# Kernel tuning notes

Measured on AMD Instinct MI355X. Metric: run time of the kernel, lower is better.

The kernel has to match this reference:

```python
import jax, jax.numpy as jnp
import numpy as np

B, N, NP, NS = 8, 4096, 1024, 32
CF = 64            # input point-feature channels; in_channel = 3 + CF = 67
MLP = [64, 128, 256]
EPS = 1e-5         # BatchNorm eps (torch default)


def setup_inputs() -> dict:
    key = jax.random.key(0)
    ks = jax.random.split(key, 8)
    inp = {
        "xyz": jax.random.normal(ks[0], (B, N, 3), jnp.float32),
        "points": jax.random.normal(ks[1], (B, CF, N), jnp.float32),
        "sample_idx": jax.random.randint(ks[2], (B, NP), 0, N, dtype=jnp.int32),
        "neighbor_idx": jax.random.randint(ks[3], (B, NP, NS), 0, N, dtype=jnp.int32),
    }
    c = 3 + CF
    for i, o in enumerate(MLP):
        wk = jax.random.fold_in(ks[4], i)
        inp[f"W{i}"] = jax.random.normal(wk, (o, c), jnp.float32) * (1.0 / np.sqrt(c))
        inp[f"b{i}"] = jnp.zeros((o,), jnp.float32)
        inp[f"gamma{i}"] = jnp.ones((o,), jnp.float32)
        inp[f"beta{i}"] = jnp.zeros((o,), jnp.float32)
        c = o
    return inp


def _forward(xyz, points, sample_idx, neighbor_idx, params):
    # xyz: (B,N,3)  points: (B,CF,N)
    new_xyz = jnp.take_along_axis(xyz, sample_idx[:, :, None], axis=1)        # (B,NP,3)
    nbr_xyz = jax.vmap(lambda x, idx: x[idx])(xyz, neighbor_idx)               # (B,NP,NS,3)
    rel = nbr_xyz - new_xyz[:, :, None, :]                                     # (B,NP,NS,3)
    nbr_feat = jax.vmap(lambda f, idx: f[:, idx])(points, neighbor_idx)        # (B,CF,NP,NS)
    x = jnp.concatenate([rel.transpose(0, 3, 1, 2), nbr_feat], axis=1)         # (B,3+CF,NP,NS)
    # 1x1 Conv2d -> BatchNorm2d (training-mode batch stats) -> ReLU stack
    for W, b, g, be in params:
        x = jnp.einsum('oc,bcps->bops', W, x) + b[None, :, None, None]
        mu = x.mean(axis=(0, 2, 3), keepdims=True)
        var = x.var(axis=(0, 2, 3), keepdims=True)
        x = g[None, :, None, None] * (x - mu) * jax.lax.rsqrt(var + EPS) + be[None, :, None, None]
        x = jax.nn.relu(x)
    new_points = x.max(axis=-1)                                                # (B,C_out,NP)
    return new_xyz, new_points


def reference(xyz, points, sample_idx, neighbor_idx,
              W0, b0, gamma0, beta0,
              W1, b1, gamma1, beta1,
              W2, b2, gamma2, beta2):
    params = [(W0, b0, gamma0, beta0), (W1, b1, gamma1, beta1), (W2, b2, gamma2, beta2)]
    return _forward(xyz, points, sample_idx, neighbor_idx, params)
```

## Files before the change

### kernel.cpp

```cpp
#include <hip/hip_runtime.h>

typedef unsigned short u16;
typedef unsigned int u32;
typedef __attribute__((ext_vector_type(8))) short short8;
typedef __attribute__((ext_vector_type(4))) float f32x4;

#define BB 8
#define NN 4096
#define NPP 1024
#define NSS 32
#define CFF 64
#define C0 67
#define H0 64
#define H1 128
#define H2 256
#define MTOT (BB*NPP*NSS)
#define BN_EPS 1e-5f
#define INV_M (1.0f/262144.0f)

#define MFMA16(a,b,c) __builtin_amdgcn_mfma_f32_16x16x32_bf16(a,b,c,0,0,0)

__device__ __forceinline__ float bf2f(u16 h){ return __uint_as_float(((u32)h)<<16); }
__device__ __forceinline__ u16 f2bf(float f){
  u32 u = __float_as_uint(f);
  u32 r = (u + 0x7fffu + ((u>>16)&1u)) >> 16;
  return (u16)r;
}
__device__ __forceinline__ u32 pack2(float a, float b){
  return (u32)f2bf(a) | ((u32)f2bf(b)<<16);
}

#define WS_NEED 46280704u

__global__ __launch_bounds__(256) void k_setup(
    const float* __restrict__ xyz, const float* __restrict__ points,
    const int* __restrict__ sidx,
    const float* __restrict__ W0, const float* __restrict__ W1, const float* __restrict__ W2,
    u16* __restrict__ ptsT, u16* __restrict__ Wt0c, u16* __restrict__ Wt1c,
    u16* __restrict__ Wt2c, float* __restrict__ out_newxyz)
{
  int blk = blockIdx.x, tid = threadIdx.x;
  if (blk < 512) {
    __shared__ float t[64][65];
    int b = blk >> 6, n0 = (blk & 63) << 6;
    int nloc = tid & 63, cpart = tid >> 6;
    for (int i = 0; i < 16; ++i) {
      int c = i*4 + cpart;
      t[c][nloc] = points[(size_t)(b*CFF + c)*NN + n0 + nloc];
    }
    __syncthreads();
    int cloc = tid & 63, npart = tid >> 6;
    for (int i = 0; i < 16; ++i) {
      int n = i*4 + npart;
      ptsT[((size_t)(b*NN + n0 + n))*CFF + cloc] = f2bf(t[cloc][n]);
    }
  } else if (blk < 544) {
    int t0 = (blk - 512)*256 + tid;
    int b = t0 >> 10;
    int s = sidx[t0];
    for (int k = 0; k < 3; ++k)
      out_newxyz[(size_t)t0*3 + k] = xyz[((size_t)(b*NN + s))*3 + k];
  } else if (blk == 544) {
    for (int i = 0; i < 24; ++i) {
      int e = i*256 + tid;
      int kc = e >> 9, o = (e >> 3) & 63, j = e & 7, k = kc*8 + j;
      float v = (k < 64) ? W0[o*C0 + 3 + k] : ((k < 67) ? W0[o*C0 + (k - 64)] : 0.f);
      Wt0c[e] = f2bf(v);
    }
  } else if (blk == 545) {
    for (int i = 0; i < 32; ++i) {
      int e = i*256 + tid;
      int kc = e >> 10, n = (e >> 3) & 127, j = e & 7;
      Wt1c[e] = f2bf(W1[n*H0 + kc*8 + j]);
    }
  } else {
    int base = (blk - 546) * 4096;
    for (int i = 0; i < 16; ++i) {
      int e = base + i*256 + tid;
      int kc = e >> 11, n = (e >> 3) & 255, j = e & 7;
      Wt2c[e] = f2bf(W2[n*H1 + kc*8 + j]);
    }
  }
}

__global__ __launch_bounds__(256) void k_xyz_only(
    const float* __restrict__ xyz, const int* __restrict__ sidx, float* __restrict__ out_newxyz)
{
  int t0 = blockIdx.x*256 + threadIdx.x;
  int b = t0 >> 10;
  int s = sidx[t0];
  for (int k = 0; k < 3; ++k)
    out_newxyz[(size_t)t0*3 + k] = xyz[((size_t)(b*NN + s))*3 + k];
}

__global__ __launch_bounds__(256) void k_l0(
    const float* __restrict__ xyz, const int* __restrict__ sidx, const int* __restrict__ nidx,
    const u16* __restrict__ ptsT, const u16* __restrict__ Wt0c,
    u16* __restrict__ y0, float* __restrict__ stats)
{
  __shared__ u16 XLc[12*512];
  __shared__ u16 W0c[12*512];
  int tid = threadIdx.x;
  int m0 = blockIdx.x * 64;
  int b = m0 >> 15;

  for (int i = 0; i < 3; ++i)
    ((uint4*)W0c)[i*256 + tid] = ((const uint4*)Wt0c)[i*256 + tid];

  int pos = tid & 63, grp = tid >> 6;
  int m = m0 + pos;
  int nb = nidx[m];
  {
    const u16* prow = ptsT + ((size_t)(b*NN + nb))*CFF + grp*16;
    uint4 h0 = *(const uint4*)prow;
    uint4 h1 = *(const uint4*)(prow + 8);
    *(uint4*)&XLc[(2*grp)*512 + pos*8]   = h0;
    *(uint4*)&XLc[(2*grp+1)*512 + pos*8] = h1;
    if (grp == 0) {
      int p = (m & 32767) >> 5;
      int sp = sidx[b*NPP + p];
      float r0 = xyz[((size_t)(b*NN+nb))*3+0] - xyz[((size_t)(b*NN+sp))*3+0];
      float r1 = xyz[((size_t)(b*NN+nb))*3+1] - xyz[((size_t)(b*NN+sp))*3+1];
      float r2 = xyz[((size_t)(b*NN+nb))*3+2] - xyz[((size_t)(b*NN+sp))*3+2];
      uint4 v = { pack2(r0, r1), pack2(r2, 0.f), 0u, 0u };
      *(uint4*)&XLc[8*512 + pos*8] = v;
    } else {
      uint4 z = {0u,0u,0u,0u};
      *(uint4*)&XLc[(8+grp)*512 + pos*8] = z;
    }
  }
  __syncthreads();

  int lane = tid & 63, wv = tid >> 6;
  int quad = lane >> 4, l15 = lane & 15;
  f32x4 acc0[4];
  for (int mi = 0; mi < 4; ++mi) acc0[mi] = (f32x4){0.f,0.f,0.f,0.f};

  for (int kc = 0; kc < 3; ++kc) {
    int cb = kc*4 + quad;
    short8 bfrag = *(const short8*)&W0c[(cb*64 + wv*16 + l15)*8];
    for (int mi = 0; mi < 4; ++mi) {
      short8 afrag = *(const short8*)&XLc[(cb*64 + mi*16 + l15)*8];
      acc0[mi] = MFMA16(afrag, bfrag, acc0[mi]);
    }
  }

  float s = 0.f, q = 0.f;
  for (int mi = 0; mi < 4; ++mi)
    for (int r = 0; r < 4; ++r) { float y = acc0[mi][r]; s += y; q += y*y; }
  s += __shfl_xor(s, 16); s += __shfl_xor(s, 32);
  q += __shfl_xor(q, 16); q += __shfl_xor(q, 32);
  if (lane < 16) {
    int slot = blockIdx.x & 7;
    atomicAdd(&stats[slot*256 + wv*16 + lane], s);
    atomicAdd(&stats[2048 + slot*256 + wv*16 + lane], q);
  }
  for (int mi = 0; mi < 4; ++mi)
    for (int r = 0; r < 4; ++r) {
      int row = m0 + mi*16 + quad*4 + r;
      y0[(size_t)row*H0 + wv*16 + l15] = f2bf(acc0[mi][r]);
    }
}

__global__ __launch_bounds__(256) void k_l1s(
    const u16* __restrict__ y0, const u16* __restrict__ Wt1c,
    const float* __restrict__ g0, const float* __restrict__ e0,
    const float* __restrict__ stIn, float* __restrict__ stOut)
{
  __shared__ u16 X0c[8*512];
  __shared__ u16 W1c[8*1024];
  __shared__ float scl0[64], sft0[64];
  int tid = threadIdx.x;
  int m0 = blockIdx.x * 64;

  if (tid < 64) {
    float s = 0.f, q = 0.f;
    for (int sl = 0; sl < 8; ++sl) { s += stIn[sl*256 + tid]; q += stIn[2048 + sl*256 + tid]; }
    float mu = s*INV_M, var = q*INV_M - mu*mu;
    float sc = g0[tid] * rsqrtf(var + BN_EPS);
    scl0[tid] = sc; sft0[tid] = e0[tid] - mu*sc;
  }
  for (int i = 0; i < 4; ++i)
    ((uint4*)W1c)[i*256 + tid] = ((const uint4*)Wt1c)[i*256 + tid];

  int pos = tid & 63, grp = tid >> 6;
  {
    const u16* row = y0 + (size_t)(m0 + pos)*H0 + grp*16;
    u16 hs[16];
    *(uint4*)&hs[0] = *(const uint4*)row;
    *(uint4*)&hs[8] = *(const uint4*)(row + 8);
    __syncthreads();
    u16 ob[16];
    for (int j = 0; j < 16; ++j) {
      int c = grp*16 + j;
      ob[j] = f2bf(fmaxf(fmaf(scl0[c], bf2f(hs[j]), sft0[c]), 0.f));
    }
    *(uint4*)&X0c[(2*grp)*512 + pos*8]   = *(uint4*)&ob[0];
    *(uint4*)&X0c[(2*grp+1)*512 + pos*8] = *(uint4*)&ob[8];
  }
  __syncthreads();

  int lane = tid & 63, wv = tid >> 6, quad = lane >> 4, l15 = lane & 15;
  f32x4 acc1[2][4];
  for (int ni = 0; ni < 2; ++ni) for (int mi = 0; mi < 4; ++mi) acc1[ni][mi] = (f32x4){0.f,0.f,0.f,0.f};

  for (int kc = 0; kc < 2; ++kc) {
    int cb = kc*4 + quad;
    short8 a[4], bfr[2];
    for (int mi = 0; mi < 4; ++mi) a[mi] = *(const short8*)&X0c[(cb*64 + mi*16 + l15)*8];
    for (int ni = 0; ni < 2; ++ni) bfr[ni] = *(const short8*)&W1c[(cb*128 + wv*32 + ni*16 + l15)*8];
    for (int ni = 0; ni < 2; ++ni)
      for (int mi = 0; mi < 4; ++mi)
        acc1[ni][mi] = MFMA16(a[mi], bfr[ni], acc1[ni][mi]);
  }

  int slot = blockIdx.x & 7;
  for (int ni = 0; ni < 2; ++ni) {
    float s = 0.f, q = 0.f;
    for (int mi = 0; mi < 4; ++mi)
      for (int r = 0; r < 4; ++r) { float y = acc1[ni][mi][r]; s += y; q += y*y; }
    s += __shfl_xor(s, 16); s += __shfl_xor(s, 32);
    q += __shfl_xor(q, 16); q += __shfl_xor(q, 32);
    if (lane < 16) {
      atomicAdd(&stOut[slot*256 + wv*32 + ni*16 + lane], s);
      atomicAdd(&stOut[2048 + slot*256 + wv*32 + ni*16 + lane], q);
    }
  }
}

__global__ __launch_bounds__(256) void k_l2f(
    const u16* __restrict__ y0, const u16* __restrict__ Wt1c, const u16* __restrict__ Wt2c,
    const float* __restrict__ g0, const float* __restrict__ e0,
    const float* __restrict__ g1, const float* __restrict__ e1,
    const float* __restrict__ st0, const float* __restrict__ st1, float* __restrict__ stOut,
    u16* __restrict__ mxp, u16* __restrict__ mnp)
{
  __shared__ u16 X1c[16*512];
  __shared__ u16 UB[16*1024];
  __shared__ float scl0[64], sft0[64], scl1[128], sft1[128];
  int tid = threadIdx.x;
  int m0 = blockIdx.x * 64;

  if (tid < 64) {
    float s = 0.f, q = 0.f;
    for (int sl = 0; sl < 8; ++sl) { s += st0[sl*256 + tid]; q += st0[2048 + sl*256 + tid]; }
    float mu = s*INV_M, var = q*INV_M - mu*mu;
    float sc = g0[tid] * rsqrtf(var + BN_EPS);
    scl0[tid] = sc; sft0[tid] = e0[tid] - mu*sc;
  }
  if (tid < 128) {
    float s = 0.f, q = 0.f;
    for (int sl = 0; sl < 8; ++sl) { s += st1[sl*256 + tid]; q += st1[2048 + sl*256 + tid]; }
    float mu = s*INV_M, var = q*INV_M - mu*mu;
    float sc = g1[tid] * rsqrtf(var + BN_EPS);
    scl1[tid] = sc; sft1[tid] = e1[tid] - mu*sc;
  }
  u16* X0c = UB;
  u16* W1c = UB + 4096;
  for (int i = 0; i < 4; ++i)
    ((uint4*)W1c)[i*256 + tid] = ((const uint4*)Wt1c)[i*256 + tid];

  int pos = tid & 63, grp = tid >> 6;
  {
    const u16* row = y0 + (size_t)(m0 + pos)*H0 + grp*16;
    u16 hs[16];
    *(uint4*)&hs[0] = *(const uint4*)row;
    *(uint4*)&hs[8] = *(const uint4*)(row + 8);
    __syncthreads();
    u16 ob[16];
    for (int j = 0; j < 16; ++j) {
      int c = grp*16 + j;
      ob[j] = f2bf(fmaxf(fmaf(scl0[c], bf2f(hs[j]), sft0[c]), 0.f));
    }
    *(uint4*)&X0c[(2*grp)*512 + pos*8]   = *(uint4*)&ob[0];
    *(uint4*)&X0c[(2*grp+1)*512 + pos*8] = *(uint4*)&ob[8];
  }
  __syncthreads();

  int lane = tid & 63, wv = tid >> 6, quad = lane >> 4, l15 = lane & 15;
  f32x4 acc1[2][4];
  for (int ni = 0; ni < 2; ++ni) for (int mi = 0; mi < 4; ++mi) acc1[ni][mi] = (f32x4){0.f,0.f,0.f,0.f};

  for (int kc = 0; kc < 2; ++kc) {
    int cb = kc*4 + quad;
    short8 a[4], bfr[2];
    for (int mi = 0; mi < 4; ++mi) a[mi] = *(const short8*)&X0c[(cb*64 + mi*16 + l15)*8];
    for (int ni = 0; ni < 2; ++ni) bfr[ni] = *(const short8*)&W1c[(cb*128 + wv*32 + ni*16 + l15)*8];
    for (int ni = 0; ni < 2; ++ni)
      for (int mi = 0; mi < 4; ++mi)
        acc1[ni][mi] = MFMA16(a[mi], bfr[ni], acc1[ni][mi]);
  }
  __syncthreads();

  for (int ni = 0; ni < 2; ++ni)
    for (int mi = 0; mi < 4; ++mi)
      for (int r = 0; r < 4; ++r) {
        int ch = wv*32 + ni*16 + l15;
        int mm = mi*16 + quad*4 + r;
        float v = fmaxf(fmaf(scl1[ch], acc1[ni][mi][r], sft1[ch]), 0.f);
        X1c[(ch >> 3)*512 + mm*8 + (ch & 7)] = f2bf(v);
      }

  f32x4 acc2[4][4];
  for (int ni = 0; ni < 4; ++ni) for (int mi = 0; mi < 4; ++mi) acc2[ni][mi] = (f32x4){0.f,0.f,0.f,0.f};

  for (int h = 0; h < 2; ++h) {
    for (int i = 0; i < 8; ++i)
      ((uint4*)UB)[i*256 + tid] = ((const uint4*)(Wt2c + h*16384))[i*256 + tid];
    __syncthreads();
    for (int kc = 0; kc < 2; ++kc) {
      int cb = kc*4 + quad;
      int cx = h*8 + cb;
      short8 a[4], bfr[4];
      for (int mi = 0; mi < 4; ++mi) a[mi] = *(const short8*)&X1c[(cx*64 + mi*16 + l15)*8];
      for (int ni = 0; ni < 4; ++ni) bfr[ni] = *(const short8*)&UB[(cb*256 + wv*64 + ni*16 + l15)*8];
      for (int ni = 0; ni < 4; ++ni)
        for (int mi = 0; mi < 4; ++mi)
          acc2[ni][mi] = MFMA16(a[mi], bfr[ni], acc2[ni][mi]);
    }
    __syncthreads();
  }

  int slot = blockIdx.x & 7;
  for (int ni = 0; ni < 4; ++ni) {
    float s = 0.f, q = 0.f;
    float mx0 = -1e30f, mn0 = 1e30f, mx1 = -1e30f, mn1 = 1e30f;
    for (int mi = 0; mi < 4; ++mi)
      for (int r = 0; r < 4; ++r) {
        float y = acc2[ni][mi][r];
        s += y; q += y*y;
        if (mi < 2) { mx0 = fmaxf(mx0, y); mn0 = fminf(mn0, y); }
        else        { mx1 = fmaxf(mx1, y); mn1 = fminf(mn1, y); }
      }
    s += __shfl_xor(s, 16); s += __shfl_xor(s, 32);
    q += __shfl_xor(q, 16); q += __shfl_xor(q, 32);
    mx0 = fmaxf(mx0, __shfl_xor(mx0, 16)); mx0 = fmaxf(mx0, __shfl_xor(mx0, 32));
    mn0 = fminf(mn0, __shfl_xor(mn0, 16)); mn0 = fminf(mn0, __shfl_xor(mn0, 32));
    mx1 = fmaxf(mx1, __shfl_xor(mx1, 16)); mx1 = fmaxf(mx1, __shfl_xor(mx1, 32));
    mn1 = fminf(mn1, __shfl_xor(mn1, 16)); mn1 = fminf(mn1, __shfl_xor(mn1, 32));
    if (lane < 16) {
      int c = wv*64 + ni*16 + lane;
      atomicAdd(&stOut[slot*256 + c], s);
      atomicAdd(&stOut[2048 + slot*256 + c], q);
      size_t pr0 = (size_t)blockIdx.x*2, pr1 = pr0 + 1;
      mxp[pr0*H2 + c] = f2bf(mx0);
      mnp[pr0*H2 + c] = f2bf(mn0);
      mxp[pr1*H2 + c] = f2bf(mx1);
      mnp[pr1*H2 + c] = f2bf(mn1);
    }
  }
}

__global__ __launch_bounds__(256) void k_final(
    const u16* __restrict__ mxp, const u16* __restrict__ mnp,
    const float* __restrict__ gma, const float* __restrict__ bta,
    const float* __restrict__ stIn, float* __restrict__ out_np)
{
  __shared__ float tmp[256][33];
  int tid = threadIdx.x;
  int b = blockIdx.x >> 5;
  int p0 = (blockIdx.x & 31) * 32;

  float s = 0.f, q = 0.f;
  for (int sl = 0; sl < 8; ++sl) { s += stIn[sl*256 + tid]; q += stIn[2048 + sl*256 + tid]; }
  float mu = s*INV_M, var = q*INV_M - mu*mu;
  float sc = gma[tid] * rsqrtf(var + BN_EPS);
  float sh = bta[tid] - mu*sc;

  for (int pp = 0; pp < 32; ++pp) {
    size_t base = ((size_t)(b*NPP + p0 + pp))*H2 + tid;
    float xv = bf2f(mxp[base]), nv = bf2f(mnp[base]);
    float v = (sc >= 0.f) ? fmaf(sc, xv, sh) : fmaf(sc, nv, sh);
    tmp[tid][pp] = fmaxf(v, 0.f);
  }
  __syncthreads();

  int pl = tid & 31, cg = tid >> 5;
  for (int cc = 0; cc < 32; ++cc) {
    int c = cc*8 + cg;
    out_np[((size_t)b*H2 + c)*NPP + p0 + pl] = tmp[c][pl];
  }
}

extern "C" void kernel_launch(void* const* d_in, const int* in_sizes, int n_in,
                              void* d_out, int out_size, void* d_ws, size_t ws_size,
                              hipStream_t stream)
{
  const float* xyz    = (const float*)d_in[0];
  const float* points = (const float*)d_in[1];
  const int*   sidx   = (const int*)d_in[2];
  const int*   nidx   = (const int*)d_in[3];
  const float* W0 = (const float*)d_in[4];
  const float* g0 = (const float*)d_in[6];
  const float* e0 = (const float*)d_in[7];
  const float* W1 = (const float*)d_in[8];
  const float* g1 = (const float*)d_in[10];
  const float* e1 = (const float*)d_in[11];
  const float* W2 = (const float*)d_in[12];
  const float* g2 = (const float*)d_in[14];
  const float* e2 = (const float*)d_in[15];

  float* out_xyz = (float*)d_out;
  float* out_np  = out_xyz + (size_t)BB*NPP*3;

  if (ws_size < (size_t)WS_NEED) {
    hipMemsetAsync(out_np, 0, (size_t)BB*H2*NPP*4, stream);
    k_xyz_only<<<32, 256, 0, stream>>>(xyz, sidx, out_xyz);
    return;
  }

  char* ws = (char*)d_ws;
  float* stats = (float*)(ws + 0);
  u16*   Wt0c  = (u16*)(ws + 49152);
  u16*   Wt1c  = (u16*)(ws + 61440);
  u16*   Wt2c  = (u16*)(ws + 77824);
  u16*   ptsT  = (u16*)(ws + 143360);
  u16*   y0    = (u16*)(ws + 4337664);
  u16*   mxp   = (u16*)(ws + 37892096);
  u16*   mnp   = (u16*)(ws + 42086400);

  hipMemsetAsync(stats, 0, 3*4096*sizeof(float), stream);
  k_setup<<<554, 256, 0, stream>>>(xyz, points, sidx, W0, W1, W2,
                                   ptsT, Wt0c, Wt1c, Wt2c, out_xyz);
  k_l0<<<MTOT/64, 256, 0, stream>>>(xyz, sidx, nidx, ptsT, Wt0c, y0, stats);
  k_l1s<<<MTOT/64, 256, 0, stream>>>(y0, Wt1c, g0, e0, stats, stats + 4096);
  k_l2f<<<MTOT/64, 256, 0, stream>>>(y0, Wt1c, Wt2c, g0, e0, g1, e1,
                                     stats, stats + 4096, stats + 8192, mxp, mnp);
  k_final<<<256, 256, 0, stream>>>(mxp, mnp, g2, e2, stats + 8192, out_np);
}
```

Measured before the change: 184.0 us.

## Switch MLP GEMMs to 32x32x16 MFMA and double rows per block in L0/L1

Replaces the 16x16x32 bf16 MFMA tiles with 32x32x16 tiles in all three layer kernels, which changes the LDS chunk layouts, the fragment indexing and the epilogue row mapping. The layer-0 and layer-1 stats kernels now handle 128 rows per block instead of 64, so half as many blocks are launched and fewer stats atomics are issued. Larger MFMA tiles do more work per instruction and need fewer shuffle reductions. The cost is more accumulator registers per wave, which may reduce occupancy.

```diff
diff --git a/kernel.cpp b/kernel.cpp
--- a/kernel.cpp
+++ b/kernel.cpp
@@ -3,7 +3,7 @@
 typedef unsigned short u16;
 typedef unsigned int u32;
 typedef __attribute__((ext_vector_type(8))) short short8;
-typedef __attribute__((ext_vector_type(4))) float f32x4;
+typedef __attribute__((ext_vector_type(16))) float f32x16;
 
 #define BB 8
 #define NN 4096
@@ -18,7 +18,7 @@
 #define BN_EPS 1e-5f
 #define INV_M (1.0f/262144.0f)
 
-#define MFMA16(a,b,c) __builtin_amdgcn_mfma_f32_16x16x32_bf16(a,b,c,0,0,0)
+#define MFMA32(a,b,c) __builtin_amdgcn_mfma_f32_32x32x16_bf16(a,b,c,0,0,0)
 
 __device__ __forceinline__ float bf2f(u16 h){ return __uint_as_float(((u32)h)<<16); }
 __device__ __forceinline__ u16 f2bf(float f){
@@ -98,67 +98,70 @@
     const u16* __restrict__ ptsT, const u16* __restrict__ Wt0c,
     u16* __restrict__ y0, float* __restrict__ stats)
 {
-  __shared__ u16 XLc[12*512];
-  __shared__ u16 W0c[12*512];
+  __shared__ u16 XLc[12*128*8];
+  __shared__ u16 W0c[12*64*8];
   int tid = threadIdx.x;
-  int m0 = blockIdx.x * 64;
+  int m0 = blockIdx.x * 128;
   int b = m0 >> 15;
 
   for (int i = 0; i < 3; ++i)
     ((uint4*)W0c)[i*256 + tid] = ((const uint4*)Wt0c)[i*256 + tid];
 
-  int pos = tid & 63, grp = tid >> 6;
+  int pos = tid & 127, half = tid >> 7;
   int m = m0 + pos;
   int nb = nidx[m];
   {
-    const u16* prow = ptsT + ((size_t)(b*NN + nb))*CFF + grp*16;
-    uint4 h0 = *(const uint4*)prow;
-    uint4 h1 = *(const uint4*)(prow + 8);
-    *(uint4*)&XLc[(2*grp)*512 + pos*8]   = h0;
-    *(uint4*)&XLc[(2*grp+1)*512 + pos*8] = h1;
-    if (grp == 0) {
+    const uint4* prow = (const uint4*)(ptsT + ((size_t)(b*NN + nb))*CFF + half*32);
+    uint4 h0 = prow[0], h1 = prow[1], h2 = prow[2], h3 = prow[3];
+    *(uint4*)&XLc[((half*4+0)*128 + pos)*8] = h0;
+    *(uint4*)&XLc[((half*4+1)*128 + pos)*8] = h1;
+    *(uint4*)&XLc[((half*4+2)*128 + pos)*8] = h2;
+    *(uint4*)&XLc[((half*4+3)*128 + pos)*8] = h3;
+    if (half == 0) {
       int p = (m & 32767) >> 5;
       int sp = sidx[b*NPP + p];
       float r0 = xyz[((size_t)(b*NN+nb))*3+0] - xyz[((size_t)(b*NN+sp))*3+0];
       float r1 = xyz[((size_t)(b*NN+nb))*3+1] - xyz[((size_t)(b*NN+sp))*3+1];
       float r2 = xyz[((size_t)(b*NN+nb))*3+2] - xyz[((size_t)(b*NN+sp))*3+2];
       uint4 v = { pack2(r0, r1), pack2(r2, 0.f), 0u, 0u };
-      *(uint4*)&XLc[8*512 + pos*8] = v;
+      *(uint4*)&XLc[(8*128 + pos)*8] = v;
     } else {
       uint4 z = {0u,0u,0u,0u};
-      *(uint4*)&XLc[(8+grp)*512 + pos*8] = z;
+      *(uint4*)&XLc[(9*128 + pos)*8]  = z;
+      *(uint4*)&XLc[(10*128 + pos)*8] = z;
+      *(uint4*)&XLc[(11*128 + pos)*8] = z;
     }
   }
   __syncthreads();
 
   int lane = tid & 63, wv = tid >> 6;
-  int quad = lane >> 4, l15 = lane & 15;
-  f32x4 acc0[4];
-  for (int mi = 0; mi < 4; ++mi) acc0[mi] = (f32x4){0.f,0.f,0.f,0.f};
-
-  for (int kc = 0; kc < 3; ++kc) {
-    int cb = kc*4 + quad;
-    short8 bfrag = *(const short8*)&W0c[(cb*64 + wv*16 + l15)*8];
-    for (int mi = 0; mi < 4; ++mi) {
-      short8 afrag = *(const short8*)&XLc[(cb*64 + mi*16 + l15)*8];
-      acc0[mi] = MFMA16(afrag, bfrag, acc0[mi]);
+  int l31 = lane & 31, kh = lane >> 5;
+  int nt = wv & 1, mtb = (wv >> 1) * 2;
+  f32x16 acc[2];
+  for (int mi = 0; mi < 2; ++mi) for (int r = 0; r < 16; ++r) acc[mi][r] = 0.f;
+
+  for (int kt = 0; kt < 6; ++kt) {
+    int ck = kt*2 + kh;
+    short8 bfrag = *(const short8*)&W0c[(ck*64 + nt*32 + l31)*8];
+    for (int mi = 0; mi < 2; ++mi) {
+      short8 afrag = *(const short8*)&XLc[(ck*128 + (mtb+mi)*32 + l31)*8];
+      acc[mi] = MFMA32(afrag, bfrag, acc[mi]);
     }
   }
 
   float s = 0.f, q = 0.f;
-  for (int mi = 0; mi < 4; ++mi)
-    for (int r = 0; r < 4; ++r) { float y = acc0[mi][r]; s += y; q += y*y; }
-  s += __shfl_xor(s, 16); s += __shfl_xor(s, 32);
-  q += __shfl_xor(q, 16); q += __shfl_xor(q, 32);
-  if (lane < 16) {
+  for (int mi = 0; mi < 2; ++mi)
+    for (int r = 0; r < 16; ++r) { float y = acc[mi][r]; s += y; q += y*y; }
+  s += __shfl_xor(s, 32); q += __shfl_xor(q, 32);
+  if (lane < 32) {
     int slot = blockIdx.x & 7;
-    atomicAdd(&stats[slot*256 + wv*16 + lane], s);
-    atomicAdd(&stats[2048 + slot*256 + wv*16 + lane], q);
-  }
-  for (int mi = 0; mi < 4; ++mi)
-    for (int r = 0; r < 4; ++r) {
-      int row = m0 + mi*16 + quad*4 + r;
-      y0[(size_t)row*H0 + wv*16 + l15] = f2bf(acc0[mi][r]);
+    atomicAdd(&stats[slot*256 + nt*32 + lane], s);
+    atomicAdd(&stats[2048 + slot*256 + nt*32 + lane], q);
+  }
+  for (int mi = 0; mi < 2; ++mi)
+    for (int r = 0; r < 16; ++r) {
+      int mm = (mtb+mi)*32 + (r&3) + 8*(r>>2) + 4*kh;
+      y0[(size_t)(m0+mm)*H0 + nt*32 + l31] = f2bf(acc[mi][r]);
     }
 }
 
@@ -167,11 +170,11 @@
     const float* __restrict__ g0, const float* __restrict__ e0,
     const float* __restrict__ stIn, float* __restrict__ stOut)
 {
-  __shared__ u16 X0c[8*512];
-  __shared__ u16 W1c[8*1024];
+  __shared__ u16 X0c[8*128*8];
+  __shared__ u16 W1c[8*128*8];
   __shared__ float scl0[64], sft0[64];
   int tid = threadIdx.x;
-  int m0 = blockIdx.x * 64;
+  int m0 = blockIdx.x * 128;
 
   if (tid < 64) {
     float s = 0.f, q = 0.f;
@@ -183,48 +186,44 @@
   for (int i = 0; i < 4; ++i)
     ((uint4*)W1c)[i*256 + tid] = ((const uint4*)Wt1c)[i*256 + tid];
 
-  int pos = tid & 63, grp = tid >> 6;
+  int pos = tid & 127, half = tid >> 7;
   {
-    const u16* row = y0 + (size_t)(m0 + pos)*H0 + grp*16;
-    u16 hs[16];
-    *(uint4*)&hs[0] = *(const uint4*)row;
-    *(uint4*)&hs[8] = *(const uint4*)(row + 8);
+    const u16* row = y0 + (size_t)(m0 + pos)*H0 + half*32;
+    u16 hs[32];
+    for (int t = 0; t < 4; ++t) *(uint4*)&hs[t*8] = ((const uint4*)row)[t];
     __syncthreads();
-    u16 ob[16];
-    for (int j = 0; j < 16; ++j) {
-      int c = grp*16 + j;
+    u16 ob[32];
+    for (int j = 0; j < 32; ++j) {
+      int c = half*32 + j;
       ob[j] = f2bf(fmaxf(fmaf(scl0[c], bf2f(hs[j]), sft0[c]), 0.f));
     }
-    *(uint4*)&X0c[(2*grp)*512 + pos*8]   = *(uint4*)&ob[0];
-    *(uint4*)&X0c[(2*grp+1)*512 + pos*8] = *(uint4*)&ob[8];
+    for (int t = 0; t < 4; ++t)
+      *(uint4*)&X0c[((half*4+t)*128 + pos)*8] = *(uint4*)&ob[t*8];
   }
   __syncthreads();
 
-  int lane = tid & 63, wv = tid >> 6, quad = lane >> 4, l15 = lane & 15;
-  f32x4 acc1[2][4];
-  for (int ni = 0; ni < 2; ++ni) for (int mi = 0; mi < 4; ++mi) acc1[ni][mi] = (f32x4){0.f,0.f,0.f,0.f};
-
-  for (int kc = 0; kc < 2; ++kc) {
-    int cb = kc*4 + quad;
-    short8 a[4], bfr[2];
-    for (int mi = 0; mi < 4; ++mi) a[mi] = *(const short8*)&X0c[(cb*64 + mi*16 + l15)*8];
-    for (int ni = 0; ni < 2; ++ni) bfr[ni] = *(const short8*)&W1c[(cb*128 + wv*32 + ni*16 + l15)*8];
-    for (int ni = 0; ni < 2; ++ni)
-      for (int mi = 0; mi < 4; ++mi)
-        acc1[ni][mi] = MFMA16(a[mi], bfr[ni], acc1[ni][mi]);
-  }
-
-  int slot = blockIdx.x & 7;
-  for (int ni = 0; ni < 2; ++ni) {
-    float s = 0.f, q = 0.f;
-    for (int mi = 0; mi < 4; ++mi)
-      for (int r = 0; r < 4; ++r) { float y = acc1[ni][mi][r]; s += y; q += y*y; }
-    s += __shfl_xor(s, 16); s += __shfl_xor(s, 32);
-    q += __shfl_xor(q, 16); q += __shfl_xor(q, 32);
-    if (lane < 16) {
-      atomicAdd(&stOut[slot*256 + wv*32 + ni*16 + lane], s);
-      atomicAdd(&stOut[2048 + slot*256 + wv*32 + ni*16 + lane], q);
-    }
+  int lane = tid & 63, wv = tid >> 6;
+  int l31 = lane & 31, kh = lane >> 5;
+  f32x16 acc[4];
+  for (int mt = 0; mt < 4; ++mt) for (int r = 0; r < 16; ++r) acc[mt][r] = 0.f;
+
+  for (int kt = 0; kt < 4; ++kt) {
+    int ck = kt*2 + kh;
+    short8 bfrag = *(const short8*)&W1c[(ck*128 + wv*32 + l31)*8];
+    for (int mt = 0; mt < 4; ++mt) {
+      short8 afrag = *(const short8*)&X0c[(ck*128 + mt*32 + l31)*8];
+      acc[mt] = MFMA32(afrag, bfrag, acc[mt]);
+    }
+  }
+
+  float s = 0.f, q = 0.f;
+  for (int mt = 0; mt < 4; ++mt)
+    for (int r = 0; r < 16; ++r) { float y = acc[mt][r]; s += y; q += y*y; }
+  s += __shfl_xor(s, 32); q += __shfl_xor(q, 32);
+  if (lane < 32) {
+    int slot = blockIdx.x & 7;
+    atomicAdd(&stOut[slot*256 + wv*32 + lane], s);
+    atomicAdd(&stOut[2048 + slot*256 + wv*32 + lane], q);
   }
 }
 
@@ -235,8 +234,8 @@
     const float* __restrict__ st0, const float* __restrict__ st1, float* __restrict__ stOut,
     u16* __restrict__ mxp, u16* __restrict__ mnp)
 {
-  __shared__ u16 X1c[16*512];
-  __shared__ u16 UB[16*1024];
+  __shared__ u16 X1c[16*64*8];
+  __shared__ u16 UB[16384];
   __shared__ float scl0[64], sft0[64], scl1[128], sft1[128];
   int tid = threadIdx.x;
   int m0 = blockIdx.x * 64;
@@ -264,89 +263,90 @@
   {
     const u16* row = y0 + (size_t)(m0 + pos)*H0 + grp*16;
     u16 hs[16];
-    *(uint4*)&hs[0] = *(const uint4*)row;
-    *(uint4*)&hs[8] = *(const uint4*)(row + 8);
+    *(uint4*)&hs[0] = ((const uint4*)row)[0];
+    *(uint4*)&hs[8] = ((const uint4*)row)[1];
     __syncthreads();
     u16 ob[16];
     for (int j = 0; j < 16; ++j) {
       int c = grp*16 + j;
       ob[j] = f2bf(fmaxf(fmaf(scl0[c], bf2f(hs[j]), sft0[c]), 0.f));
     }
-    *(uint4*)&X0c[(2*grp)*512 + pos*8]   = *(uint4*)&ob[0];
-    *(uint4*)&X0c[(2*grp+1)*512 + pos*8] = *(uint4*)&ob[8];
+    *(uint4*)&X0c[((2*grp)*64 + pos)*8]   = *(uint4*)&ob[0];
+    *(uint4*)&X0c[((2*grp+1)*64 + pos)*8] = *(uint4*)&ob[8];
   }
   __syncthreads();
 
-  int lane = tid & 63, wv = tid >> 6, quad = lane >> 4, l15 = lane & 15;
-  f32x4 acc1[2][4];
-  for (int ni = 0; ni < 2; ++ni) for (int mi = 0; mi < 4; ++mi) acc1[ni][mi] = (f32x4){0.f,0.f,0.f,0.f};
-
-  for (int kc = 0; kc < 2; ++kc) {
-    int cb = kc*4 + quad;
-    short8 a[4], bfr[2];
-    for (int mi = 0; mi < 4; ++mi) a[mi] = *(const short8*)&X0c[(cb*64 + mi*16 + l15)*8];
-    for (int ni = 0; ni < 2; ++ni) bfr[ni] = *(const short8*)&W1c[(cb*128 + wv*32 + ni*16 + l15)*8];
-    for (int ni = 0; ni < 2; ++ni)
-      for (int mi = 0; mi < 4; ++mi)
-        acc1[ni][mi] = MFMA16(a[mi], bfr[ni], acc1[ni][mi]);
+  int lane = tid & 63, wv = tid >> 6;
+  int l31 = lane & 31, kh = lane >> 5;
+
+  f32x16 acc1[2];
+  for (int mt = 0; mt < 2; ++mt) for (int r = 0; r < 16; ++r) acc1[mt][r] = 0.f;
+  for (int kt = 0; kt < 4; ++kt) {
+    int ck = kt*2 + kh;
+    short8 bfrag = *(const short8*)&W1c[(ck*128 + wv*32 + l31)*8];
+    for (int mt = 0; mt < 2; ++mt) {
+      short8 afrag = *(const short8*)&X0c[(ck*64 + mt*32 + l31)*8];
+      acc1[mt] = MFMA32(afrag, bfrag, acc1[mt]);
+    }
+  }
+
+  {
+    int ch = wv*32 + l31;
+    int cb = ch >> 3, cr = ch & 7;
+    float sc1 = scl1[ch], sf1 = sft1[ch];
+    for (int mt = 0; mt < 2; ++mt)
+      for (int r = 0; r < 16; ++r) {
+        int mm = mt*32 + (r&3) + 8*(r>>2) + 4*kh;
+        X1c[(cb*64 + mm)*8 + cr] = f2bf(fmaxf(fmaf(sc1, acc1[mt][r], sf1), 0.f));
+      }
   }
   __syncthreads();
 
-  for (int ni = 0; ni < 2; ++ni)
-    for (int mi = 0; mi < 4; ++mi)
-      for (int r = 0; r < 4; ++r) {
-        int ch = wv*32 + ni*16 + l15;
-        int mm = mi*16 + quad*4 + r;
-        float v = fmaxf(fmaf(scl1[ch], acc1[ni][mi][r], sft1[ch]), 0.f);
-        X1c[(ch >> 3)*512 + mm*8 + (ch & 7)] = f2bf(v);
-      }
-
-  f32x4 acc2[4][4];
-  for (int ni = 0; ni < 4; ++ni) for (int mi = 0; mi < 4; ++mi) acc2[ni][mi] = (f32x4){0.f,0.f,0.f,0.f};
+  f32x16 acc2[2][2];
+  for (int nt = 0; nt < 2; ++nt) for (int mt = 0; mt < 2; ++mt)
+    for (int r = 0; r < 16; ++r) acc2[nt][mt][r] = 0.f;
 
   for (int h = 0; h < 2; ++h) {
     for (int i = 0; i < 8; ++i)
-      ((uint4*)UB)[i*256 + tid] = ((const uint4*)(Wt2c + h*16384))[i*256 + tid];
+      ((uint4*)UB)[i*256 + tid] = ((const uint4*)Wt2c)[h*2048 + i*256 + tid];
     __syncthreads();
-    for (int kc = 0; kc < 2; ++kc) {
-      int cb = kc*4 + quad;
-      int cx = h*8 + cb;
-      short8 a[4], bfr[4];
-      for (int mi = 0; mi < 4; ++mi) a[mi] = *(const short8*)&X1c[(cx*64 + mi*16 + l15)*8];
-      for (int ni = 0; ni < 4; ++ni) bfr[ni] = *(const short8*)&UB[(cb*256 + wv*64 + ni*16 + l15)*8];
-      for (int ni = 0; ni < 4; ++ni)
-        for (int mi = 0; mi < 4; ++mi)
-          acc2[ni][mi] = MFMA16(a[mi], bfr[ni], acc2[ni][mi]);
+    for (int k4 = 0; k4 < 4; ++k4) {
+      int ckx = (h*4 + k4)*2 + kh;
+      int ckw = k4*2 + kh;
+      short8 a[2], bf_[2];
+      for (int mt = 0; mt < 2; ++mt) a[mt]  = *(const short8*)&X1c[(ckx*64 + mt*32 + l31)*8];
+      for (int nt = 0; nt < 2; ++nt) bf_[nt] = *(const short8*)&UB[(ckw*256 + wv*64 + nt*32 + l31)*8];
+      for (int nt = 0; nt < 2; ++nt)
+        for (int mt = 0; mt < 2; ++mt)
+          acc2[nt][mt] = MFMA32(a[mt], bf_[nt], acc2[nt][mt]);
     }
     __syncthreads();
   }
 
   int slot = blockIdx.x & 7;
-  for (int ni = 0; ni < 4; ++ni) {
+  for (int nt = 0; nt < 2; ++nt) {
     float s = 0.f, q = 0.f;
-    float mx0 = -1e30f, mn0 = 1e30f, mx1 = -1e30f, mn1 = 1e30f;
-    for (int mi = 0; mi < 4; ++mi)
-      for (int r = 0; r < 4; ++r) {
-        float y = acc2[ni][mi][r];
+    float mx[2] = {-3.0e38f, -3.0e38f}, mn[2] = {3.0e38f, 3.0e38f};
+    for (int mt = 0; mt < 2; ++mt)
+      for (int r = 0; r < 16; ++r) {
+        float y = acc2[nt][mt][r];
         s += y; q += y*y;
-        if (mi < 2) { mx0 = fmaxf(mx0, y); mn0 = fminf(mn0, y); }
-        else        { mx1 = fmaxf(mx1, y); mn1 = fminf(mn1, y); }
+        mx[mt] = fmaxf(mx[mt], y); mn[mt] = fminf(mn[mt], y);
       }
-    s += __shfl_xor(s, 16); s += __shfl_xor(s, 32);
-    q += __shfl_xor(q, 16); q += __shfl_xor(q, 32);
-    mx0 = fmaxf(mx0, __shfl_xor(mx0, 16)); mx0 = fmaxf(mx0, __shfl_xor(mx0, 32));
-    mn0 = fminf(mn0, __shfl_xor(mn0, 16)); mn0 = fminf(mn0, __shfl_xor(mn0, 32));
-    mx1 = fmaxf(mx1, __shfl_xor(mx1, 16)); mx1 = fmaxf(mx1, __shfl_xor(mx1, 32));
-    mn1 = fminf(mn1, __shfl_xor(mn1, 16)); mn1 = fminf(mn1, __shfl_xor(mn1, 32));
-    if (lane < 16) {
-      int c = wv*64 + ni*16 + lane;
+    s += __shfl_xor(s, 32); q += __shfl_xor(q, 32);
+    mx[0] = fmaxf(mx[0], __shfl_xor(mx[0], 32));
+    mx[1] = fmaxf(mx[1], __shfl_xor(mx[1], 32));
+    mn[0] = fminf(mn[0], __shfl_xor(mn[0], 32));
+    mn[1] = fminf(mn[1], __shfl_xor(mn[1], 32));
+    if (lane < 32) {
+      int c = wv*64 + nt*32 + lane;
       atomicAdd(&stOut[slot*256 + c], s);
       atomicAdd(&stOut[2048 + slot*256 + c], q);
-      size_t pr0 = (size_t)blockIdx.x*2, pr1 = pr0 + 1;
-      mxp[pr0*H2 + c] = f2bf(mx0);
-      mnp[pr0*H2 + c] = f2bf(mn0);
-      mxp[pr1*H2 + c] = f2bf(mx1);
-      mnp[pr1*H2 + c] = f2bf(mn1);
+      for (int mt = 0; mt < 2; ++mt) {
+        size_t pr = (size_t)blockIdx.x*2 + mt;
+        mxp[pr*H2 + c] = f2bf(mx[mt]);
+        mnp[pr*H2 + c] = f2bf(mn[mt]);
+      }
     }
   }
 }
@@ -422,8 +422,8 @@
   hipMemsetAsync(stats, 0, 3*4096*sizeof(float), stream);
   k_setup<<<554, 256, 0, stream>>>(xyz, points, sidx, W0, W1, W2,
                                    ptsT, Wt0c, Wt1c, Wt2c, out_xyz);
-  k_l0<<<MTOT/64, 256, 0, stream>>>(xyz, sidx, nidx, ptsT, Wt0c, y0, stats);
-  k_l1s<<<MTOT/64, 256, 0, stream>>>(y0, Wt1c, g0, e0, stats, stats + 4096);
+  k_l0<<<MTOT/128, 256, 0, stream>>>(xyz, sidx, nidx, ptsT, Wt0c, y0, stats);
+  k_l1s<<<MTOT/128, 256, 0, stream>>>(y0, Wt1c, g0, e0, stats, stats + 4096);
   k_l2f<<<MTOT/64, 256, 0, stream>>>(y0, Wt1c, Wt2c, g0, e0, g1, e1,
                                      stats, stats + 4096, stats + 8192, mxp, mnp);
   k_final<<<256, 256, 0, stream>>>(mxp, mnp, g2, e2, stats + 8192, out_np);
```

Result: faster. 178.6 us (-3.0%).
